# Kernel optimization log

Measured on AMD Instinct MI355X. Metric: run time of the kernel, lower is better.

## Reference

```python
import jax, jax.numpy as jnp
import numpy as np

RANK = 2
ALPHA = 0.1
BASE_SCALE = 500.0
HIDDEN = 512
INPUT = 8
NUM_MIX = 2
NUM_SEEDS = 4
BATCH = 64
SEQ = 2048
D = 2 * RANK + INPUT  # 12


def setup_inputs() -> dict:
    key = jax.random.key(0)
    k1, k2, k3, k4 = jax.random.split(key, 4)
    x = jax.random.normal(k1, (BATCH, SEQ, INPUT), dtype=jnp.float32)
    means = jnp.zeros((NUM_MIX, D), dtype=jnp.float32)
    # mirror torch init: covariance (hence tril) scaled ~ 1/sqrt(hidden_size)
    scale_tril = jax.random.normal(k2, (NUM_MIX, D, D), dtype=jnp.float32) / jnp.sqrt(jnp.float32(HIDDEN))
    mixture_weights = jnp.ones((NUM_MIX,), dtype=jnp.float32)
    seeds = jax.random.normal(k3, (NUM_SEEDS, HIDDEN, D), dtype=jnp.float32)
    cur_seeds = jax.random.randint(k4, (BATCH,), 0, NUM_SEEDS, dtype=jnp.int32)
    return {"x": x, "means": means, "scale_tril": scale_tril,
            "mixture_weights": mixture_weights, "seeds": seeds, "cur_seeds": cur_seeds}


def _clamp_tril(scale_tril):
    # lower-triangular with strictly positive diagonal (matches _clamp_tril)
    diag = jnp.abs(jnp.diagonal(scale_tril, axis1=-2, axis2=-1) - 1e-12) + 1e-12
    return jnp.tril(scale_tril, -1) + jax.vmap(jnp.diag)(diag)


def reference(x, means, scale_tril, mixture_weights, seeds, cur_seeds):
    L = _clamp_tril(scale_tril)                       # (M, D, D)
    w = jnp.clip(mixture_weights, 1e-6, None)
    w = w / jnp.sum(w)                                # normalized mixture weights

    # samp[i, s, h, :] = means[i] + L[i] @ seeds[s, h]
    samp = jnp.einsum('ide,she->ishd', L, seeds) + means[:, None, None, :]
    comb = jnp.einsum('i,ishd->shd', w, samp)         # weighted mixture sum, (S, H, D)
    m = comb[..., :RANK]                              # (S, H, r)
    n = comb[..., RANK:2 * RANK]                      # (S, H, r)
    I = comb[..., 2 * RANK:]                          # (S, H, in)

    J = jnp.einsum('shr,sgr->shg', m, n) * (BASE_SCALE / HIDDEN)   # (S, H, H)

    Jb = J[cur_seeds]                                 # (B, H, H) per-sample recurrence matrix
    Ib = I[cur_seeds]                                 # (B, H, in)
    Ix = jnp.einsum('bhi,bti->bth', Ib, x)            # precomputed input injection (B, T, H)

    def step(h, ix_t):
        dh = -h + jnp.einsum('bhg,bg->bh', Jb, jnp.tanh(h)) + ix_t
        h = h + ALPHA * dh
        return h, h

    h0 = jnp.zeros((x.shape[0], HIDDEN), dtype=x.dtype)
    _, hiddens = jax.lax.scan(step, h0, jnp.swapaxes(Ix, 0, 1))    # (T, B, H)
    hiddens = jnp.swapaxes(hiddens, 0, 1)             # (B, T, H)

    # down_project=True: project onto span([m, I]) via pinv per seed
    span = jnp.concatenate([m, I], axis=-1)           # (S, H, r+in)
    pinv = jnp.linalg.pinv(span)                      # (S, r+in, H)
    out = jnp.einsum('bkh,bth->btk', pinv[cur_seeds], hiddens)     # (B, T, r+in)
    return out
```

## Files before the change

kernel.cpp:

```cpp
#include <hip/hip_runtime.h>
#include <math.h>

#define HIDDEN  512
#define INPUT   8
#define NUM_MIX 2
#define BATCH   64
#define SEQ     2048
#define DD      12
#define KOUT    10
#define TTILE   16
#define NTILES  (SEQ/TTILE)

#define SCALE_F 2.8853900817779268
#define AB_F    0.09765625f

typedef float v2f __attribute__((ext_vector_type(2)));
typedef float f4v __attribute__((ext_vector_type(4)));
typedef unsigned int v2u __attribute__((ext_vector_type(2)));

__device__ __forceinline__ v2f pk_fma(v2f a, v2f b, v2f c) {
    return __builtin_elementwise_fma(a, b, c);
}

template<int CTRL>
__device__ __forceinline__ float dpp_add(float x) {
    int y = __builtin_amdgcn_update_dpp(0, __float_as_int(x), CTRL, 0xF, 0xF, true);
    return x + __int_as_float(y);
}
__device__ __forceinline__ float wave_allsum(float x) {
    x = dpp_add<0x111>(x);
    x = dpp_add<0x112>(x);
    x = dpp_add<0x114>(x);
    x = dpp_add<0x118>(x);
    x = dpp_add<0x142>(x);
    x = dpp_add<0x143>(x);
    return __int_as_float(__builtin_amdgcn_readlane(__float_as_int(x), 63));
}

__device__ __forceinline__ void allsum2(float p0, float p1,
                                        float& v0, float& v1) {
#if __has_builtin(__builtin_amdgcn_permlane32_swap)
    v2u sw = __builtin_amdgcn_permlane32_swap(
        __float_as_uint(p0), __float_as_uint(p1), false, false);
    float z = __uint_as_float(sw.x) + __uint_as_float(sw.y);
    z = dpp_add<0x111>(z);
    z = dpp_add<0x112>(z);
    z = dpp_add<0x114>(z);
    z = dpp_add<0x118>(z);
    z = dpp_add<0x142>(z);
    v0 = __int_as_float(__builtin_amdgcn_readlane(__float_as_int(z), 31));
    v1 = __int_as_float(__builtin_amdgcn_readlane(__float_as_int(z), 63));
#else
    v0 = wave_allsum(p0);
    v1 = wave_allsum(p1);
#endif
}

__global__ __launch_bounds__(256) void fsm_rnn_kernel(
    const float* __restrict__ x,
    const float* __restrict__ means,
    const float* __restrict__ scale_tril,
    const float* __restrict__ mixw,
    const float* __restrict__ seeds,
    const int*   __restrict__ cur_seeds,
    float*       __restrict__ out)
{
    __shared__ __align__(16) float IxP[2][TTILE][4][64][2];
    __shared__ __align__(16) float xsB[2][TTILE*INPUT];
    __shared__ __align__(16) float IvL[HIDDEN][INPUT];
    __shared__ float PM0[HIDDEN], PM1[HIDDEN], N0[HIDDEN], N1[HIDDEN];
    __shared__ __align__(8) float vr2[2][TTILE][64][2];
    __shared__ double Leff[DD*DD];
    __shared__ double meansw[DD];

    const int tid  = threadIdx.x;
    const int lane = tid & 63;
    const int wid  = tid >> 6;
    const int b    = blockIdx.x;
    const int s    = cur_seeds[b];
    const float* xb = x + (size_t)b * SEQ * INPUT;
    float* outb = out + (size_t)b * SEQ * KOUT;

    double w0 = fmax((double)mixw[0], 1e-6);
    double w1 = fmax((double)mixw[1], 1e-6);
    double wsum = w0 + w1; w0 /= wsum; w1 /= wsum;

    if (tid < DD*DD) {
        int d = tid / DD, e = tid % DD;
        double acc = 0.0;
        #pragma unroll
        for (int i = 0; i < NUM_MIX; ++i) {
            float v = scale_tril[i*DD*DD + d*DD + e];
            float c = (d > e) ? v : (d == e ? fabsf(v - 1e-12f) + 1e-12f : 0.0f);
            acc += (i == 0 ? w0 : w1) * (double)c;
        }
        Leff[tid] = acc;
    }
    if (tid < DD)
        meansw[tid] = w0 * (double)means[tid] + w1 * (double)means[DD + tid];
    if (tid < 2*TTILE*INPUT)
        ((float*)xsB)[tid] = xb[tid];
    __syncthreads();

    #pragma unroll
    for (int rr = 0; rr < 2; ++rr) {
        int h = tid + rr*256;
        const float* sh = &seeds[(s*HIDDEN + h)*DD];
        double comb[DD];
        #pragma unroll
        for (int d = 0; d < DD; ++d) {
            double acc = meansw[d];
            for (int e = 0; e <= d; ++e)
                acc += Leff[d*DD + e] * (double)sh[e];
            comb[d] = acc;
        }
        PM0[h] = (float)(SCALE_F * (double)AB_F * comb[0]);
        PM1[h] = (float)(SCALE_F * (double)AB_F * comb[1]);
        N0[h]  = (float)comb[2];
        N1[h]  = (float)comb[3];
        #pragma unroll
        for (int i = 0; i < INPUT; ++i)
            IvL[h][i] = (float)(SCALE_F * 0.1 * comb[4 + i]);
    }
    __syncthreads();

    v2f AM0[4], AM1[4], NN0v[4], NN1v[4], H[4];
    f4v IvA[3], IvC[3];
    float zf = 0.0f, wst = 0.0f;
    const int pid = (wid - 1)*64 + lane;
    const int zi  = lane - 56;

    if (wid == 0) {
        #pragma unroll
        for (int q = 0; q < 4; ++q) {
            int ha = lane + 64*(2*q), hb = lane + 64*(2*q + 1);
            AM0[q]  = (v2f){PM0[ha], PM0[hb]};
            AM1[q]  = (v2f){PM1[ha], PM1[hb]};
            NN0v[q] = (v2f){N0[ha],  N0[hb]};
            NN1v[q] = (v2f){N1[ha],  N1[hb]};
            H[q]    = (v2f){0.0f, 0.0f};
        }
    } else {
        #pragma unroll
        for (int q = 0; q < 3; ++q) {
            int h = pid + 192*q;
            if (h < HIDDEN) {
                IvA[q] = *(const f4v*)&IvL[h][0];
                IvC[q] = *(const f4v*)&IvL[h][4];
            }
        }
    }

    auto produce = [&](int tg) {
        const int pb = tg & 1;
        const float* xs = xsB[pb];
        for (int tt = 0; tt < TTILE; ++tt) {
            f4v xa = *(const f4v*)&xs[tt*INPUT];
            f4v xc = *(const f4v*)&xs[tt*INPUT + 4];
            #pragma unroll
            for (int q = 0; q < 3; ++q) {
                int h = pid + 192*q;
                if (h < HIDDEN) {
                    float v =      IvA[q].x * xa.x;
                    v = fmaf(IvA[q].y, xa.y, v);
                    v = fmaf(IvA[q].z, xa.z, v);
                    v = fmaf(IvA[q].w, xa.w, v);
                    v = fmaf(IvC[q].x, xc.x, v);
                    v = fmaf(IvC[q].y, xc.y, v);
                    v = fmaf(IvC[q].z, xc.z, v);
                    v = fmaf(IvC[q].w, xc.w, v);
                    IxP[pb][tt][(h >> 7)][h & 63][(h >> 6) & 1] = v;
                }
            }
        }
        if (wid == 1 && lane >= 56) {
            #pragma unroll 4
            for (int tt = 0; tt < TTILE; ++tt) {
                zf = fmaf(0.9f, zf, 0.1f * xs[tt*INPUT + zi]);
                outb[(tg*TTILE + tt)*KOUT + 2 + zi] = zf;
            }
        }
    };

    auto process_w = [&](int tile) {
        if (lane == 54 || lane == 55) {
            const int widx = lane & 1;
            for (int tt = 0; tt < TTILE; ++tt) {
                wst = fmaf(0.9f, wst, AB_F * vr2[tile & 1][tt][0][widx]);
                outb[(tile*TTILE + tt)*KOUT + widx] = wst;
            }
        }
    };

    if (wid != 0) produce(0);
    __syncthreads();

    for (int T = 0; T < NTILES; ++T) {
        if (wid == 0) {
            const int pb = T & 1;
            v2f CC[4], CN[4];
            #pragma unroll
            for (int q = 0; q < 4; ++q)
                CC[q] = *(const v2f*)&IxP[pb][0][q][lane][0];
            #pragma unroll
            for (int tt = 0; tt < TTILE; ++tt) {
                if (tt < TTILE-1) {
                    #pragma unroll
                    for (int q = 0; q < 4; ++q)
                        CN[q] = *(const v2f*)&IxP[pb][tt+1][q][lane][0];
                }
                v2f TH[4];
                #pragma unroll
                for (int q = 0; q < 4; ++q) {
                    v2f E;
                    E.x = __builtin_amdgcn_exp2f(H[q].x);
                    E.y = __builtin_amdgcn_exp2f(H[q].y);
                    v2f A = E + 1.0f;
                    v2f R;
                    R.x = __builtin_amdgcn_rcpf(A.x);
                    R.y = __builtin_amdgcn_rcpf(A.y);
                    const v2f m2 = {-2.0f, -2.0f}, one = {1.0f, 1.0f};
                    TH[q] = pk_fma(m2, R, one);
                }
                v2f s0 = TH[0]*NN0v[0];
                s0 = pk_fma(TH[1], NN0v[1], s0);
                s0 = pk_fma(TH[2], NN0v[2], s0);
                s0 = pk_fma(TH[3], NN0v[3], s0);
                v2f s1 = TH[0]*NN1v[0];
                s1 = pk_fma(TH[1], NN1v[1], s1);
                s1 = pk_fma(TH[2], NN1v[2], s1);
                s1 = pk_fma(TH[3], NN1v[3], s1);
                float p0 = s0.x + s0.y;
                float p1 = s1.x + s1.y;

                float v0, v1;
                allsum2(p0, p1, v0, v1);

                const v2f nine = {0.9f, 0.9f};
                v2f hc0 = pk_fma(nine, H[0], CC[0]);
                v2f hc1 = pk_fma(nine, H[1], CC[1]);
                v2f hc2 = pk_fma(nine, H[2], CC[2]);
                v2f hc3 = pk_fma(nine, H[3], CC[3]);

                v2f v0v = {v0, v0}, v1v = {v1, v1};
                H[0] = pk_fma(AM0[0], v0v, pk_fma(AM1[0], v1v, hc0));
                H[1] = pk_fma(AM0[1], v0v, pk_fma(AM1[1], v1v, hc1));
                H[2] = pk_fma(AM0[2], v0v, pk_fma(AM1[2], v1v, hc2));
                H[3] = pk_fma(AM0[3], v0v, pk_fma(AM1[3], v1v, hc3));

                *(v2f*)&vr2[pb][tt][lane][0] = (v2f){v0, v1};

                #pragma unroll
                for (int q = 0; q < 4; ++q) CC[q] = CN[q];
            }
        } else {
            if (T + 1 < NTILES) produce(T + 1);
            if (wid == 2 && T + 2 < NTILES) {
                const int base = (T + 2)*(TTILE*INPUT);
                xsB[T & 1][lane]      = xb[base + lane];
                xsB[T & 1][lane + 64] = xb[base + lane + 64];
            }
            if (wid == 1 && T >= 1) process_w(T - 1);
        }
        __syncthreads();
    }
    if (wid == 1) process_w(NTILES - 1);
}

extern "C" void kernel_launch(void* const* d_in, const int* in_sizes, int n_in,
                              void* d_out, int out_size, void* d_ws, size_t ws_size,
                              hipStream_t stream) {
    (void)d_ws; (void)ws_size;
    const float* x          = (const float*)d_in[0];
    const float* means      = (const float*)d_in[1];
    const float* scale_tril = (const float*)d_in[2];
    const float* mixw       = (const float*)d_in[3];
    const float* seeds      = (const float*)d_in[4];
    const int*   cur_seeds  = (const int*)d_in[5];
    float* out = (float*)d_out;

    fsm_rnn_kernel<<<BATCH, 256, 0, stream>>>(
        x, means, scale_tril, mixw, seeds, cur_seeds, out);
}
```

Before: 459.8 us.

## Break serial recurrence dependency with linearized one-step lookahead of rank-2 state

The rank-2 recurrence now evaluates tanh at an extrapolated hidden state (2*v_cur - v_prev) and also accumulates a Jacobian-like 2x2 matrix (sech^2 weighted) alongside the usual projection. The next step's projected values are then reconstructed with a first-order Taylor correction instead of waiting on the cross-lane reduction. The aim is to take the wave-wide allsum off the critical serial path so that reductions overlap with the next step's math. In exchange each step does three allsum2 reductions instead of one plus extra FMAs, and the result is approximate: the linearization error could accumulate over 2048 steps.

```diff
diff --git a/kernel.cpp b/kernel.cpp
--- a/kernel.cpp
+++ b/kernel.cpp
@@ -12,6 +12,7 @@
 #define NTILES  (SEQ/TTILE)
 
 #define SCALE_F 2.8853900817779268
+#define INVS_F  0.34657359027997264f
 #define AB_F    0.09765625f
 
 typedef float v2f __attribute__((ext_vector_type(2)));
@@ -124,7 +125,11 @@
     }
     __syncthreads();
 
-    v2f AM0[4], AM1[4], NN0v[4], NN1v[4], H[4];
+    v2f AM0[4], AM1[4], N0v[4], N1v[4];
+    v2f C00[4], C01[4], C10[4], C11[4];
+    v2f uS[4];
+    float vc0=0.f, vc1=0.f, vp0=0.f, vp1=0.f, vh0=0.f, vh1=0.f;
+    float g0s=0.f, g1s=0.f, Gr00=0.f, Gr01=0.f, Gr10=0.f, Gr11=0.f;
     f4v IvA[3], IvC[3];
     float zf = 0.0f, wst = 0.0f;
     const int pid = (wid - 1)*64 + lane;
@@ -134,11 +139,14 @@
         #pragma unroll
         for (int q = 0; q < 4; ++q) {
             int ha = lane + 64*(2*q), hb = lane + 64*(2*q + 1);
-            AM0[q]  = (v2f){PM0[ha], PM0[hb]};
-            AM1[q]  = (v2f){PM1[ha], PM1[hb]};
-            NN0v[q] = (v2f){N0[ha],  N0[hb]};
-            NN1v[q] = (v2f){N1[ha],  N1[hb]};
-            H[q]    = (v2f){0.0f, 0.0f};
+            AM0[q] = (v2f){PM0[ha], PM0[hb]};
+            AM1[q] = (v2f){PM1[ha], PM1[hb]};
+            N0v[q] = (v2f){N0[ha],  N0[hb]};
+            N1v[q] = (v2f){N1[ha],  N1[hb]};
+            v2f a0n = AM0[q] * INVS_F, a1n = AM1[q] * INVS_F;
+            C00[q] = N0v[q] * a0n;  C01[q] = N0v[q] * a1n;
+            C10[q] = N1v[q] * a0n;  C11[q] = N1v[q] * a1n;
+            uS[q]  = (v2f){0.0f, 0.0f};
         }
     } else {
         #pragma unroll
@@ -209,49 +217,60 @@
                     for (int q = 0; q < 4; ++q)
                         CN[q] = *(const v2f*)&IxP[pb][tt+1][q][lane][0];
                 }
-                v2f TH[4];
+                float d0 = vc0 - vh0, d1 = vc1 - vh1;
+                float vn0 = fmaf(Gr00, d0, fmaf(Gr01, d1, g0s));
+                float vn1 = fmaf(Gr10, d0, fmaf(Gr11, d1, g1s));
+                *(v2f*)&vr2[pb][tt][lane][0] = (v2f){vn0, vn1};
+
+                float nh0 = fmaf(2.0f, vc0, -vp0);
+                float nh1 = fmaf(2.0f, vc1, -vp1);
+                v2f vcv0 = {vc0, vc0}, vcv1 = {vc1, vc1};
+                v2f vhv0 = {nh0, nh0}, vhv1 = {nh1, nh1};
+                v2f sg0, sg1, s00, s01, s10, s11;
                 #pragma unroll
                 for (int q = 0; q < 4; ++q) {
-                    v2f E;
-                    E.x = __builtin_amdgcn_exp2f(H[q].x);
-                    E.y = __builtin_amdgcn_exp2f(H[q].y);
-                    v2f A = E + 1.0f;
-                    v2f R;
+                    v2f Hq = pk_fma(AM0[q], vcv0, pk_fma(AM1[q], vcv1, uS[q]));
+                    v2f uq = pk_fma((v2f){0.9f,0.9f}, Hq, CC[q]);
+                    uS[q] = uq;
+                    v2f Hh = pk_fma(AM0[q], vhv0, pk_fma(AM1[q], vhv1, uq));
+                    v2f E, A, R, Th, Sh;
+                    E.x = __builtin_amdgcn_exp2f(Hh.x);
+                    E.y = __builtin_amdgcn_exp2f(Hh.y);
+                    A = E + 1.0f;
                     R.x = __builtin_amdgcn_rcpf(A.x);
                     R.y = __builtin_amdgcn_rcpf(A.y);
-                    const v2f m2 = {-2.0f, -2.0f}, one = {1.0f, 1.0f};
-                    TH[q] = pk_fma(m2, R, one);
+                    Th = pk_fma((v2f){-2.0f,-2.0f}, R, (v2f){1.0f,1.0f});
+                    Sh = pk_fma(-Th, Th, (v2f){1.0f,1.0f});
+                    if (q == 0) {
+                        sg0 = Th*N0v[0]; sg1 = Th*N1v[0];
+                        s00 = Sh*C00[0]; s01 = Sh*C01[0];
+                        s10 = Sh*C10[0]; s11 = Sh*C11[0];
+                    } else {
+                        sg0 = pk_fma(Th, N0v[q], sg0);
+                        sg1 = pk_fma(Th, N1v[q], sg1);
+                        s00 = pk_fma(Sh, C00[q], s00);
+                        s01 = pk_fma(Sh, C01[q], s01);
+                        s10 = pk_fma(Sh, C10[q], s10);
+                        s11 = pk_fma(Sh, C11[q], s11);
+                    }
                 }
-                v2f s0 = TH[0]*NN0v[0];
-                s0 = pk_fma(TH[1], NN0v[1], s0);
-                s0 = pk_fma(TH[2], NN0v[2], s0);
-                s0 = pk_fma(TH[3], NN0v[3], s0);
-                v2f s1 = TH[0]*NN1v[0];
-                s1 = pk_fma(TH[1], NN1v[1], s1);
-                s1 = pk_fma(TH[2], NN1v[2], s1);
-                s1 = pk_fma(TH[3], NN1v[3], s1);
-                float p0 = s0.x + s0.y;
-                float p1 = s1.x + s1.y;
-
-                float v0, v1;
-                allsum2(p0, p1, v0, v1);
-
-                const v2f nine = {0.9f, 0.9f};
-                v2f hc0 = pk_fma(nine, H[0], CC[0]);
-                v2f hc1 = pk_fma(nine, H[1], CC[1]);
-                v2f hc2 = pk_fma(nine, H[2], CC[2]);
-                v2f hc3 = pk_fma(nine, H[3], CC[3]);
-
-                v2f v0v = {v0, v0}, v1v = {v1, v1};
-                H[0] = pk_fma(AM0[0], v0v, pk_fma(AM1[0], v1v, hc0));
-                H[1] = pk_fma(AM0[1], v0v, pk_fma(AM1[1], v1v, hc1));
-                H[2] = pk_fma(AM0[2], v0v, pk_fma(AM1[2], v1v, hc2));
-                H[3] = pk_fma(AM0[3], v0v, pk_fma(AM1[3], v1v, hc3));
-
-                *(v2f*)&vr2[pb][tt][lane][0] = (v2f){v0, v1};
-
-                #pragma unroll
-                for (int q = 0; q < 4; ++q) CC[q] = CN[q];
+                float pg0 = sg0.x + sg0.y, pg1 = sg1.x + sg1.y;
+                float p00 = s00.x + s00.y, p01 = s01.x + s01.y;
+                float p10 = s10.x + s10.y, p11 = s11.x + s11.y;
+                float tg0, tg1, t00, t01, t10, t11;
+                allsum2(pg0, pg1, tg0, tg1);
+                allsum2(p00, p01, t00, t01);
+                allsum2(p10, p11, t10, t11);
+                g0s = tg0; g1s = tg1;
+                Gr00 = t00; Gr01 = t01; Gr10 = t10; Gr11 = t11;
+                vp0 = vc0; vp1 = vc1;
+                vc0 = vn0; vc1 = vn1;
+                vh0 = nh0; vh1 = nh1;
+
+                if (tt < TTILE-1) {
+                    #pragma unroll
+                    for (int q = 0; q < 4; ++q) CC[q] = CN[q];
+                }
             }
         } else {
             if (T + 1 < NTILES) produce(T + 1);
```

Measured after the change: 631.4 us. +37.3%, slower.

## Parallelize recurrence across time with linearized Newton-style correction over four waves

Applied to the files above, without the earlier changes.

Replaces the single sequential wave per tile with four evaluator waves that each take four timesteps of a 16-step tile. Each wave guesses the rank-2 state from the last known feedback, linearizes tanh around it using the derivative, and then runs a corrected second pass and a final first-order fix-up. This shortens the serial dependency chain per timestep. In exchange it adds redundant tanh evaluations, two more block barriers per tile, and a twice-larger block. Exactness is not guaranteed, since the feedback is only corrected to first order.

```diff
diff --git a/kernel.cpp b/kernel.cpp
--- a/kernel.cpp
+++ b/kernel.cpp
@@ -10,9 +10,12 @@
 #define KOUT    10
 #define TTILE   16
 #define NTILES  (SEQ/TTILE)
+#define NEV     4
+#define BLKT    512
 
 #define SCALE_F 2.8853900817779268
 #define AB_F    0.09765625f
+#define TWOLN2  1.3862943611198906f
 
 typedef float v2f __attribute__((ext_vector_type(2)));
 typedef float f4v __attribute__((ext_vector_type(4)));
@@ -56,7 +59,7 @@
 #endif
 }
 
-__global__ __launch_bounds__(256) void fsm_rnn_kernel(
+__global__ __launch_bounds__(BLKT) void fsm_rnn_kernel(
     const float* __restrict__ x,
     const float* __restrict__ means,
     const float* __restrict__ scale_tril,
@@ -69,7 +72,8 @@
     __shared__ __align__(16) float xsB[2][TTILE*INPUT];
     __shared__ __align__(16) float IvL[HIDDEN][INPUT];
     __shared__ float PM0[HIDDEN], PM1[HIDDEN], N0[HIDDEN], N1[HIDDEN];
-    __shared__ __align__(8) float vr2[2][TTILE][64][2];
+    __shared__ __align__(16) float VG[2][TTILE][8];
+    __shared__ __align__(8)  float Vfin[2][TTILE][2];
     __shared__ double Leff[DD*DD];
     __shared__ double meansw[DD];
 
@@ -102,9 +106,8 @@
         ((float*)xsB)[tid] = xb[tid];
     __syncthreads();
 
-    #pragma unroll
-    for (int rr = 0; rr < 2; ++rr) {
-        int h = tid + rr*256;
+    {
+        const int h = tid;
         const float* sh = &seeds[(s*HIDDEN + h)*DD];
         double comb[DD];
         #pragma unroll
@@ -124,56 +127,55 @@
     }
     __syncthreads();
 
-    v2f AM0[4], AM1[4], NN0v[4], NN1v[4], H[4];
-    f4v IvA[3], IvC[3];
-    float zf = 0.0f, wst = 0.0f;
-    const int pid = (wid - 1)*64 + lane;
-    const int zi  = lane - 56;
-
-    if (wid == 0) {
+    v2f AM0[4], AM1[4], N0v[4], N1v[4], C00[4], C01[4], C10[4], C11[4], Hst[4];
+    float vh0 = 0.f, vh1 = 0.f;
+    f4v IvA0{}, IvC0{}, IvA1{}, IvC1{};
+    float zf = 0.f, wst = 0.f;
+    const int zi = lane - 56;
+
+    if (wid < NEV) {
         #pragma unroll
         for (int q = 0; q < 4; ++q) {
-            int ha = lane + 64*(2*q), hb = lane + 64*(2*q + 1);
-            AM0[q]  = (v2f){PM0[ha], PM0[hb]};
-            AM1[q]  = (v2f){PM1[ha], PM1[hb]};
-            NN0v[q] = (v2f){N0[ha],  N0[hb]};
-            NN1v[q] = (v2f){N1[ha],  N1[hb]};
-            H[q]    = (v2f){0.0f, 0.0f};
+            int ha = lane + 128*q, hb = ha + 64;
+            AM0[q] = (v2f){PM0[ha], PM0[hb]};
+            AM1[q] = (v2f){PM1[ha], PM1[hb]};
+            N0v[q] = (v2f){N0[ha],  N0[hb]};
+            N1v[q] = (v2f){N1[ha],  N1[hb]};
+            C00[q] = N0v[q] * AM0[q];
+            C01[q] = N0v[q] * AM1[q];
+            C10[q] = N1v[q] * AM0[q];
+            C11[q] = N1v[q] * AM1[q];
+            Hst[q] = (v2f){0.0f, 0.0f};
         }
     } else {
-        #pragma unroll
-        for (int q = 0; q < 3; ++q) {
-            int h = pid + 192*q;
-            if (h < HIDDEN) {
-                IvA[q] = *(const f4v*)&IvL[h][0];
-                IvC[q] = *(const f4v*)&IvL[h][4];
-            }
-        }
+        const int u0 = (wid - NEV)*128 + lane;
+        IvA0 = *(const f4v*)&IvL[u0][0];
+        IvC0 = *(const f4v*)&IvL[u0][4];
+        IvA1 = *(const f4v*)&IvL[u0 + 64][0];
+        IvC1 = *(const f4v*)&IvL[u0 + 64][4];
     }
 
     auto produce = [&](int tg) {
-        const int pb = tg & 1;
-        const float* xs = xsB[pb];
+        const int pbx = tg & 1;
+        const int p = wid - NEV;
+        const float* xs = xsB[pbx];
+        #pragma unroll
         for (int tt = 0; tt < TTILE; ++tt) {
             f4v xa = *(const f4v*)&xs[tt*INPUT];
             f4v xc = *(const f4v*)&xs[tt*INPUT + 4];
-            #pragma unroll
-            for (int q = 0; q < 3; ++q) {
-                int h = pid + 192*q;
-                if (h < HIDDEN) {
-                    float v =      IvA[q].x * xa.x;
-                    v = fmaf(IvA[q].y, xa.y, v);
-                    v = fmaf(IvA[q].z, xa.z, v);
-                    v = fmaf(IvA[q].w, xa.w, v);
-                    v = fmaf(IvC[q].x, xc.x, v);
-                    v = fmaf(IvC[q].y, xc.y, v);
-                    v = fmaf(IvC[q].z, xc.z, v);
-                    v = fmaf(IvC[q].w, xc.w, v);
-                    IxP[pb][tt][(h >> 7)][h & 63][(h >> 6) & 1] = v;
-                }
-            }
-        }
-        if (wid == 1 && lane >= 56) {
+            float va = IvA0.x*xa.x;
+            va = fmaf(IvA0.y, xa.y, va); va = fmaf(IvA0.z, xa.z, va);
+            va = fmaf(IvA0.w, xa.w, va); va = fmaf(IvC0.x, xc.x, va);
+            va = fmaf(IvC0.y, xc.y, va); va = fmaf(IvC0.z, xc.z, va);
+            va = fmaf(IvC0.w, xc.w, va);
+            float vb = IvA1.x*xa.x;
+            vb = fmaf(IvA1.y, xa.y, vb); vb = fmaf(IvA1.z, xa.z, vb);
+            vb = fmaf(IvA1.w, xa.w, vb); vb = fmaf(IvC1.x, xc.x, vb);
+            vb = fmaf(IvC1.y, xc.y, vb); vb = fmaf(IvC1.z, xc.z, vb);
+            vb = fmaf(IvC1.w, xc.w, vb);
+            *(v2f*)&IxP[pbx][tt][p][lane][0] = (v2f){va, vb};
+        }
+        if (wid == NEV && lane >= 56) {
             #pragma unroll 4
             for (int tt = 0; tt < TTILE; ++tt) {
                 zf = fmaf(0.9f, zf, 0.1f * xs[tt*INPUT + zi]);
@@ -186,85 +188,170 @@
         if (lane == 54 || lane == 55) {
             const int widx = lane & 1;
             for (int tt = 0; tt < TTILE; ++tt) {
-                wst = fmaf(0.9f, wst, AB_F * vr2[tile & 1][tt][0][widx]);
+                wst = fmaf(0.9f, wst, AB_F * Vfin[tile & 1][tt][widx]);
                 outb[(tile*TTILE + tt)*KOUT + widx] = wst;
             }
         }
     };
 
-    if (wid != 0) produce(0);
+    if (wid >= NEV) produce(0);
     __syncthreads();
 
     for (int T = 0; T < NTILES; ++T) {
-        if (wid == 0) {
-            const int pb = T & 1;
-            v2f CC[4], CN[4];
-            #pragma unroll
-            for (int q = 0; q < 4; ++q)
-                CC[q] = *(const v2f*)&IxP[pb][0][q][lane][0];
-            #pragma unroll
-            for (int tt = 0; tt < TTILE; ++tt) {
-                if (tt < TTILE-1) {
+        const int pb = T & 1;
+        v2f HbOwn[4][4], HbC[4];
+        float WgA1[4], WgB1[4], WgA2[4], WgB2[4];
+        float W16a[16], W16b[16];
+
+        if (wid < NEV) {
+            v2f Hb[4] = {Hst[0], Hst[1], Hst[2], Hst[3]};
+            float Wa = 0.f, Wb = 0.f;
+            #pragma unroll
+            for (int jg = 0; jg < 4; ++jg) {
+                const bool own = (jg == wid);
+                #pragma unroll
+                for (int ii = 0; ii < 4; ++ii) {
+                    const int j = jg*4 + ii;
+                    if (own) {
+                        #pragma unroll
+                        for (int q = 0; q < 4; ++q) HbOwn[ii][q] = Hb[q];
+                        WgA1[ii] = Wa; WgB1[ii] = Wb;
+                    }
                     #pragma unroll
-                    for (int q = 0; q < 4; ++q)
-                        CN[q] = *(const v2f*)&IxP[pb][tt+1][q][lane][0];
-                }
-                v2f TH[4];
+                    for (int q = 0; q < 4; ++q) {
+                        v2f cc = *(const v2f*)&IxP[pb][j][q][lane][0];
+                        Hb[q] = pk_fma((v2f){0.9f, 0.9f}, Hb[q], cc);
+                    }
+                    Wa = fmaf(0.9f, Wa, vh0);
+                    Wb = fmaf(0.9f, Wb, vh1);
+                }
+            }
+            #pragma unroll
+            for (int q = 0; q < 4; ++q) HbC[q] = Hb[q];
+
+            #pragma unroll
+            for (int i = 0; i < 4; ++i) {
+                v2f gav = {WgA1[i], WgA1[i]}, gbv = {WgB1[i], WgB1[i]};
+                v2f pv0, pv1, pg00, pg01, pg10, pg11;
                 #pragma unroll
                 for (int q = 0; q < 4; ++q) {
-                    v2f E;
-                    E.x = __builtin_amdgcn_exp2f(H[q].x);
-                    E.y = __builtin_amdgcn_exp2f(H[q].y);
+                    v2f Hq = pk_fma(AM0[q], gav, pk_fma(AM1[q], gbv, HbOwn[i][q]));
+                    v2f E, R;
+                    E.x = __builtin_amdgcn_exp2f(Hq.x);
+                    E.y = __builtin_amdgcn_exp2f(Hq.y);
                     v2f A = E + 1.0f;
-                    v2f R;
                     R.x = __builtin_amdgcn_rcpf(A.x);
                     R.y = __builtin_amdgcn_rcpf(A.y);
-                    const v2f m2 = {-2.0f, -2.0f}, one = {1.0f, 1.0f};
-                    TH[q] = pk_fma(m2, R, one);
-                }
-                v2f s0 = TH[0]*NN0v[0];
-                s0 = pk_fma(TH[1], NN0v[1], s0);
-                s0 = pk_fma(TH[2], NN0v[2], s0);
-                s0 = pk_fma(TH[3], NN0v[3], s0);
-                v2f s1 = TH[0]*NN1v[0];
-                s1 = pk_fma(TH[1], NN1v[1], s1);
-                s1 = pk_fma(TH[2], NN1v[2], s1);
-                s1 = pk_fma(TH[3], NN1v[3], s1);
-                float p0 = s0.x + s0.y;
-                float p1 = s1.x + s1.y;
-
-                float v0, v1;
-                allsum2(p0, p1, v0, v1);
-
-                const v2f nine = {0.9f, 0.9f};
-                v2f hc0 = pk_fma(nine, H[0], CC[0]);
-                v2f hc1 = pk_fma(nine, H[1], CC[1]);
-                v2f hc2 = pk_fma(nine, H[2], CC[2]);
-                v2f hc3 = pk_fma(nine, H[3], CC[3]);
-
-                v2f v0v = {v0, v0}, v1v = {v1, v1};
-                H[0] = pk_fma(AM0[0], v0v, pk_fma(AM1[0], v1v, hc0));
-                H[1] = pk_fma(AM0[1], v0v, pk_fma(AM1[1], v1v, hc1));
-                H[2] = pk_fma(AM0[2], v0v, pk_fma(AM1[2], v1v, hc2));
-                H[3] = pk_fma(AM0[3], v0v, pk_fma(AM1[3], v1v, hc3));
-
-                *(v2f*)&vr2[pb][tt][lane][0] = (v2f){v0, v1};
-
-                #pragma unroll
-                for (int q = 0; q < 4; ++q) CC[q] = CN[q];
+                    v2f Th = pk_fma((v2f){-2.f,-2.f}, R, (v2f){1.f,1.f});
+                    v2f S2 = (E * R) * R * (v2f){TWOLN2, TWOLN2};
+                    if (q == 0) {
+                        pv0 = Th*N0v[0];  pv1 = Th*N1v[0];
+                        pg00 = S2*C00[0]; pg01 = S2*C01[0];
+                        pg10 = S2*C10[0]; pg11 = S2*C11[0];
+                    } else {
+                        pv0 = pk_fma(Th, N0v[q], pv0);
+                        pv1 = pk_fma(Th, N1v[q], pv1);
+                        pg00 = pk_fma(S2, C00[q], pg00);
+                        pg01 = pk_fma(S2, C01[q], pg01);
+                        pg10 = pk_fma(S2, C10[q], pg10);
+                        pg11 = pk_fma(S2, C11[q], pg11);
+                    }
+                }
+                float v0, v1, g00, g01, g10, g11;
+                allsum2(pv0.x + pv0.y,  pv1.x + pv1.y,  v0,  v1);
+                allsum2(pg00.x + pg00.y, pg01.x + pg01.y, g00, g01);
+                allsum2(pg10.x + pg10.y, pg11.x + pg11.y, g10, g11);
+                if (lane == 0) {
+                    const int t = wid*4 + i;
+                    *(v2f*)&VG[0][t][0] = (v2f){v0, v1};
+                    *(f4v*)&VG[0][t][4] = (f4v){g00, g01, g10, g11};
+                }
             }
         } else {
             if (T + 1 < NTILES) produce(T + 1);
-            if (wid == 2 && T + 2 < NTILES) {
+            if (wid == NEV + 1 && T + 2 < NTILES) {
                 const int base = (T + 2)*(TTILE*INPUT);
                 xsB[T & 1][lane]      = xb[base + lane];
                 xsB[T & 1][lane + 64] = xb[base + lane + 64];
             }
-            if (wid == 1 && T >= 1) process_w(T - 1);
+            if (wid == NEV && T >= 1) process_w(T - 1);
+        }
+        __syncthreads();
+
+        if (wid < NEV) {
+            float Wca = 0.f, Wcb = 0.f, Wga = 0.f, Wgb = 0.f;
+            #pragma unroll
+            for (int jg = 0; jg < 4; ++jg) {
+                const bool own = (jg == wid);
+                #pragma unroll
+                for (int ii = 0; ii < 4; ++ii) {
+                    const int t = jg*4 + ii;
+                    f4v dv = *(const f4v*)&VG[0][t][0];
+                    f4v dG = *(const f4v*)&VG[0][t][4];
+                    if (own) { WgA2[ii] = Wca; WgB2[ii] = Wcb; }
+                    float dA = Wca - Wga, dB = Wcb - Wgb;
+                    float v0f = fmaf(dG.x, dA, fmaf(dG.y, dB, dv.x));
+                    float v1f = fmaf(dG.z, dA, fmaf(dG.w, dB, dv.y));
+                    W16a[t] = Wca; W16b[t] = Wcb;
+                    Wga = fmaf(0.9f, Wga, vh0);
+                    Wgb = fmaf(0.9f, Wgb, vh1);
+                    Wca = fmaf(0.9f, Wca, v0f);
+                    Wcb = fmaf(0.9f, Wcb, v1f);
+                }
+            }
+            #pragma unroll
+            for (int i = 0; i < 4; ++i) {
+                v2f gav = {WgA2[i], WgA2[i]}, gbv = {WgB2[i], WgB2[i]};
+                v2f pv0, pv1;
+                #pragma unroll
+                for (int q = 0; q < 4; ++q) {
+                    v2f Hq = pk_fma(AM0[q], gav, pk_fma(AM1[q], gbv, HbOwn[i][q]));
+                    v2f E, R;
+                    E.x = __builtin_amdgcn_exp2f(Hq.x);
+                    E.y = __builtin_amdgcn_exp2f(Hq.y);
+                    v2f A = E + 1.0f;
+                    R.x = __builtin_amdgcn_rcpf(A.x);
+                    R.y = __builtin_amdgcn_rcpf(A.y);
+                    v2f Th = pk_fma((v2f){-2.f,-2.f}, R, (v2f){1.f,1.f});
+                    if (q == 0) { pv0 = Th*N0v[0]; pv1 = Th*N1v[0]; }
+                    else {
+                        pv0 = pk_fma(Th, N0v[q], pv0);
+                        pv1 = pk_fma(Th, N1v[q], pv1);
+                    }
+                }
+                float v0, v1;
+                allsum2(pv0.x + pv0.y, pv1.x + pv1.y, v0, v1);
+                if (lane == 0)
+                    *(v2f*)&VG[1][wid*4 + i][0] = (v2f){v0, v1};
+            }
+        }
+        __syncthreads();
+
+        if (wid < NEV) {
+            float Wca = 0.f, Wcb = 0.f;
+            float vl0 = 0.f, vl1 = 0.f;
+            #pragma unroll
+            for (int t = 0; t < TTILE; ++t) {
+                f4v dv = *(const f4v*)&VG[1][t][0];
+                f4v dG = *(const f4v*)&VG[0][t][4];
+                float dA = Wca - W16a[t], dB = Wcb - W16b[t];
+                float v0f = fmaf(dG.x, dA, fmaf(dG.y, dB, dv.x));
+                float v1f = fmaf(dG.z, dA, fmaf(dG.w, dB, dv.y));
+                if (tid == 0)
+                    *(v2f*)&Vfin[pb][t][0] = (v2f){v0f, v1f};
+                Wca = fmaf(0.9f, Wca, v0f);
+                Wcb = fmaf(0.9f, Wcb, v1f);
+                vl0 = v0f; vl1 = v1f;
+            }
+            vh0 = vl0; vh1 = vl1;
+            v2f wav = {Wca, Wca}, wbv = {Wcb, Wcb};
+            #pragma unroll
+            for (int q = 0; q < 4; ++q)
+                Hst[q] = pk_fma(AM0[q], wav, pk_fma(AM1[q], wbv, HbC[q]));
         }
         __syncthreads();
     }
-    if (wid == 1) process_w(NTILES - 1);
+    if (wid == NEV) process_w(NTILES - 1);
 }
 
 extern "C" void kernel_launch(void* const* d_in, const int* in_sizes, int n_in,
@@ -279,6 +366,6 @@
     const int*   cur_seeds  = (const int*)d_in[5];
     float* out = (float*)d_out;
 
-    fsm_rnn_kernel<<<BATCH, 256, 0, stream>>>(
+    fsm_rnn_kernel<<<BATCH, BLKT, 0, stream>>>(
         x, means, scale_tril, mixw, seeds, cur_seeds, out);
 }
```

After: 1.104 ms. 140% more time.
